# Performance work log

Hardware: AMD Instinct MI355X
Metric: run time of the kernel (lower is better)

The kernel has to match this reference:

```python
import jax, jax.numpy as jnp
import numpy as np

# Dims: B batch, CK key dim, CV value dim, NOBJ objects, T memory frames, HxW feature map
B, CK, CV, NOBJ, T, H, W = 1, 64, 512, 2, 2, 64, 64


def setup_inputs() -> dict:
    key = jax.random.key(0)
    k1, k2, k3, k4, k5 = jax.random.split(key, 5)
    return {
        "query_key": jax.random.normal(k1, (B, CK, H, W), jnp.float32),
        "query_selection": jax.random.uniform(k2, (B, CK, H, W), jnp.float32),
        "memory_key": jax.random.normal(k3, (B, CK, T, H, W), jnp.float32),
        "memory_shrinkage": jax.random.uniform(k4, (B, 1, T, H, W), jnp.float32),
        "memory_value": jax.random.normal(k5, (B, NOBJ, CV, T, H, W), jnp.float32),
    }


def reference(query_key, query_selection, memory_key, memory_shrinkage, memory_value):
    b, nobj, cv = memory_value.shape[:3]
    ck = memory_key.shape[1]
    h, w = query_key.shape[-2:]
    hw = h * w
    mk = memory_key.reshape(b, ck, -1)            # (b, ck, N) with N = T*H*W
    ms = memory_shrinkage.reshape(b, -1)          # (b, N)
    qk = query_key.reshape(b, ck, hw)             # (b, ck, hw)
    qe = query_selection.reshape(b, ck, hw)       # (b, ck, hw)
    mv = memory_value.reshape(b, nobj * cv, -1)   # (b, nobj*cv, N)

    # Negative L2 similarity with selection weighting (XMem get_similarity)
    a_sq = jnp.einsum('bcn,bcp->bnp', mk * mk, qe)            # (b, N, hw)
    two_ab = 2.0 * jnp.einsum('bcn,bcp->bnp', mk, qk * qe)    # (b, N, hw)
    b_sq = jnp.sum(qe * qk * qk, axis=1, keepdims=True)       # (b, 1, hw)
    inv_sqrt_ck = np.float32(1.0 / np.sqrt(ck))
    sim = (two_ab - a_sq - b_sq) * ms[:, :, None] * inv_sqrt_ck

    # Softmax over memory slots (dim N), then weighted readout
    aff = jax.nn.softmax(sim, axis=1)                          # (b, N, hw)
    mem = jnp.einsum('bvn,bnp->bvp', mv, aff)                  # (b, nobj*cv, hw)
    return mem.reshape(b, nobj, cv, h, w)
```

## Files before the change

kernel.cpp:

```cpp
#include <hip/hip_runtime.h>
#include <stdint.h>

typedef unsigned short u16;
typedef __attribute__((ext_vector_type(4))) float f32x4;
typedef __attribute__((ext_vector_type(8))) __bf16 bf16x8;
typedef __attribute__((ext_vector_type(4))) unsigned int u32x4;

#define HWPX 4096
#define NMEM 8192
#define CKD  64
#define VROWS 1024

__device__ __forceinline__ u16 f2bf(float x) {
    union { float f; unsigned u; } v; v.f = x;
    unsigned r = v.u + 0x7FFFu + ((v.u >> 16) & 1u);
    return (u16)(r >> 16);
}

__device__ __forceinline__ void gld_lds16(const void* g, void* l) {
    __builtin_amdgcn_global_load_lds(
        (const __attribute__((address_space(1))) uint32_t*)g,
        (__attribute__((address_space(3))) uint32_t*)l, 16, 0, 0);
}


__global__ void prep_qk(const float* __restrict__ qk, const float* __restrict__ qe,
                        const float* __restrict__ mk,
                        u16* __restrict__ Qf, float* __restrict__ bsq,
                        u16* __restrict__ Kf) {
    const int bx = blockIdx.x;
    const int tid = threadIdx.x;
    if (bx < 16) {
        int p = bx * 256 + tid;
        const int pt = p >> 7, wm = (p >> 6) & 1, mi = (p >> 4) & 3, l15 = p & 15;
        const size_t cb = ((((size_t)pt * 2 + 0) * 2 + wm) * 4 + mi) * 2;
        float acc = 0.f;
        #pragma unroll
        for (int cg = 0; cg < 8; ++cg) {
            const int kk = cg >> 2, quad = cg & 3;
            float kv[8], ev[8];
            #pragma unroll
            for (int j = 0; j < 8; ++j) {
                int c = cg * 8 + j;
                kv[j] = qk[c * HWPX + p];
                ev[j] = qe[c * HWPX + p];
                acc += ev[j] * kv[j] * kv[j];
            }
            unsigned w0[4], w1[4];
            #pragma unroll
            for (int jj = 0; jj < 4; ++jj) {
                w0[jj] = (unsigned)f2bf(kv[2*jj] * ev[2*jj]) |
                         ((unsigned)f2bf(kv[2*jj+1] * ev[2*jj+1]) << 16);
                w1[jj] = (unsigned)f2bf(ev[2*jj]) |
                         ((unsigned)f2bf(ev[2*jj+1]) << 16);
            }
            const size_t off = (size_t)quad * 128 + (size_t)l15 * 8;
            *(u32x4*)(Qf + (cb + kk) * 512 + off)      = (u32x4){w0[0], w0[1], w0[2], w0[3]};
            *(u32x4*)(Qf + (cb + 16 + kk) * 512 + off) = (u32x4){w1[0], w1[1], w1[2], w1[3]};
        }
        bsq[p] = acc;
    } else {
        int n = (bx - 16) * 256 + tid;
        const int nt = n >> 7, wn = (n >> 6) & 1, ni = (n >> 4) & 3, l15 = n & 15;
        const size_t cb = ((((size_t)nt * 2 + 0) * 2 + wn) * 4 + ni) * 2;
        #pragma unroll
        for (int cg = 0; cg < 8; ++cg) {
            const int kk = cg >> 2, quad = cg & 3;
            float m[8];
            #pragma unroll
            for (int j = 0; j < 8; ++j)
                m[j] = mk[(cg * 8 + j) * NMEM + n];
            unsigned w0[4], w1[4];
            #pragma unroll
            for (int jj = 0; jj < 4; ++jj) {
                w0[jj] = (unsigned)f2bf(2.f * m[2*jj]) |
                         ((unsigned)f2bf(2.f * m[2*jj+1]) << 16);
                w1[jj] = (unsigned)f2bf(-m[2*jj] * m[2*jj]) |
                         ((unsigned)f2bf(-m[2*jj+1] * m[2*jj+1]) << 16);
            }
            const size_t off = (size_t)quad * 128 + (size_t)l15 * 8;
            *(u32x4*)(Kf + (cb + kk) * 512 + off)      = (u32x4){w0[0], w0[1], w0[2], w0[3]};
            *(u32x4*)(Kf + (cb + 16 + kk) * 512 + off) = (u32x4){w1[0], w1[1], w1[2], w1[3]};
        }
    }
}

__launch_bounds__(256, 2)
__global__ void gemm1_combo(const u16* __restrict__ Qf, const u16* __restrict__ Kf,
                            const float* __restrict__ bsq, const float* __restrict__ ms,
                            const float* __restrict__ mv,
                            u16* __restrict__ Pt, float* __restrict__ dpart,
                            u16* __restrict__ mvb, float* __restrict__ outz) {
    const int blk = blockIdx.x;
    const int tid = threadIdx.x;

    if (blk < 512) {
        #pragma unroll 4
        for (int it = 0; it < 16; ++it) {
            int i = blk * 4096 + it * 256 + tid;
            float4 v = ((const float4*)mv)[i];
            u16 o0 = f2bf(v.x), o1 = f2bf(v.y), o2 = f2bf(v.z), o3 = f2bf(v.w);
            unsigned lo = (unsigned)o0 | ((unsigned)o1 << 16);
            unsigned hi = (unsigned)o2 | ((unsigned)o3 << 16);
            ((uint2*)mvb)[i] = make_uint2(lo, hi);
        }
        return;
    }
    if (blk < 768) {
        #pragma unroll 4
        for (int it = 0; it < 16; ++it) {
            int i = (blk - 512) * 4096 + it * 256 + tid;
            ((float4*)outz)[i] = make_float4(0.f, 0.f, 0.f, 0.f);
        }
        return;
    }

    __shared__ __align__(16) u16 smem[17408];

    const int tile = blk - 768;
    const int pb = tile & 31;
    const int nb = tile >> 5;
    const int p0 = pb * 128;
    const int n0 = nb * 128;

    const int l    = tid & 63;
    const int w    = tid >> 6;
    const int quad = l >> 4;
    const int l15  = l & 15;
    const int wm = w >> 1, wn = w & 1;

    f32x4 acc[4][4] = {};

    #pragma unroll
    for (int h = 0; h < 2; ++h) {
        bf16x8 a[4][2], b[4][2];
        const u16* qbase = Qf + ((((size_t)pb * 2 + h) * 2 + wm) * 4096) + (size_t)l * 8;
        const u16* kbase = Kf + ((((size_t)nb * 2 + h) * 2 + wn) * 4096) + (size_t)l * 8;
        #pragma unroll
        for (int mi = 0; mi < 4; ++mi) {
            a[mi][0] = *(const bf16x8*)(qbase + mi * 1024);
            a[mi][1] = *(const bf16x8*)(qbase + mi * 1024 + 512);
        }
        #pragma unroll
        for (int ni = 0; ni < 4; ++ni) {
            b[ni][0] = *(const bf16x8*)(kbase + ni * 1024);
            b[ni][1] = *(const bf16x8*)(kbase + ni * 1024 + 512);
        }
        #pragma unroll
        for (int kk = 0; kk < 2; ++kk)
            #pragma unroll
            for (int mi = 0; mi < 4; ++mi)
                #pragma unroll
                for (int ni = 0; ni < 4; ++ni)
                    acc[mi][ni] = __builtin_amdgcn_mfma_f32_16x16x32_bf16(a[mi][kk], b[ni][kk], acc[mi][ni], 0, 0, 0);
    }

    float msv[4];
    #pragma unroll
    for (int ni = 0; ni < 4; ++ni)
        msv[ni] = ms[n0 + wn * 64 + ni * 16 + l15] * 0.125f;
    float bsv[4][4];
    #pragma unroll
    for (int mi = 0; mi < 4; ++mi)
        #pragma unroll
        for (int r = 0; r < 4; ++r)
            bsv[mi][r] = bsq[p0 + wm * 64 + mi * 16 + quad * 4 + r];

    u16* Ps = smem;
    float rowsum[4][4] = {};
    #pragma unroll
    for (int mi = 0; mi < 4; ++mi) {
        #pragma unroll
        for (int ni = 0; ni < 4; ++ni) {
            f32x4 v = acc[mi][ni];
            int col = wn * 64 + ni * 16 + l15;
            #pragma unroll
            for (int r = 0; r < 4; ++r) {
                int rowl = wm * 64 + mi * 16 + quad * 4 + r;
                float pv = __expf((v[r] - bsv[mi][r]) * msv[ni]);
                rowsum[mi][r] += pv;
                Ps[rowl * 136 + col] = f2bf(pv);
            }
        }
    }
    #pragma unroll
    for (int mi = 0; mi < 4; ++mi)
        #pragma unroll
        for (int r = 0; r < 4; ++r) {
            float s = rowsum[mi][r];
            s += __shfl_xor(s, 1);
            s += __shfl_xor(s, 2);
            s += __shfl_xor(s, 4);
            s += __shfl_xor(s, 8);
            rowsum[mi][r] = s;
        }
    {
        float myv = 0.f;
        #pragma unroll
        for (int mi = 0; mi < 4; ++mi)
            #pragma unroll
            for (int r = 0; r < 4; ++r)
                if (l15 == mi * 4 + r) myv = rowsum[mi][r];
        int slice = nb * 2 + wn;
        dpart[(size_t)slice * HWPX + p0 + wm * 64 + (l15 >> 2) * 16 + quad * 4 + (l15 & 3)] = myv;
    }
    __syncthreads();

    {
        const size_t dstBase = (size_t)pb * 1048576 + (size_t)nb * 16384;
        #pragma unroll
        for (int it = 0; it < 8; ++it) {
            const int combo = it * 4 + w;
            const int kt  = combo >> 4;
            const int wnq = (combo >> 3) & 1;
            const int niq = (combo >> 1) & 3;
            const int kkq = combo & 1;
            const u32x4* src = (const u32x4*)(Ps + (wnq * 64 + niq * 16 + l15) * 136
                                                 + kt * 64 + kkq * 32 + quad * 8);
            u32x4* dst = (u32x4*)(Pt + dstBase + kt * 8192 + wnq * 4096
                                     + niq * 1024 + kkq * 512 + l * 8);
            *dst = *src;
        }
    }
}

__launch_bounds__(256, 3)
__global__ void gemm2_kernel(const u16* __restrict__ Ab, const u16* __restrict__ Btf,
                             const float* __restrict__ dpart, float* __restrict__ outacc) {
    __shared__ __align__(16) u16 As[128 * 64];

    const int tid  = threadIdx.x;
    const int l    = tid & 63;
    const int w    = tid >> 6;
    const int quad = l >> 4;
    const int l15  = l & 15;
    const int wm = w >> 1, wn = w & 1;

    const int lin = blockIdx.x + (blockIdx.y << 3) + (blockIdx.z << 8);
    const int vb  = (lin >> 3) & 7;
    const int pb  = (lin & 7) | (((lin >> 6) & 3) << 3);
    const int kz  = lin >> 8;
    const int v0 = vb * 128;
    const int p0 = pb * 128;
    const int kbeg = kz * (NMEM / 4);
    const int kend = kbeg + (NMEM / 4);

    const int rsub = tid >> 3;
    const int csw  = (tid & 7) ^ (rsub & 7);

    const u16* bbase = Btf + (size_t)pb * 1048576 + (size_t)wn * 4096 + (size_t)l * 8;

    f32x4 acc[4][4] = {};

    for (int k0 = kbeg; k0 < kend; k0 += 64) {
        const int kt = k0 >> 6;
        __syncthreads();
        #pragma unroll
        for (int rnd = 0; rnd < 4; ++rnd)
            gld_lds16(Ab + (size_t)(v0 + rnd * 32 + rsub) * NMEM + k0 + csw * 8,
                      As + rnd * 2048 + w * 512);
        bf16x8 b[4][2];
        {
            const u16* bk = bbase + (size_t)kt * 8192;
            #pragma unroll
            for (int ni = 0; ni < 4; ++ni) {
                b[ni][0] = *(const bf16x8*)(bk + ni * 1024);
                b[ni][1] = *(const bf16x8*)(bk + ni * 1024 + 512);
            }
        }
        __syncthreads();
        #pragma unroll
        for (int kk = 0; kk < 2; ++kk) {
            bf16x8 a[4];
            #pragma unroll
            for (int mi = 0; mi < 4; ++mi) {
                int row = wm * 64 + mi * 16 + l15;
                a[mi] = *(const bf16x8*)(As + row * 64 + (((kk * 4 + quad) ^ (l15 & 7)) << 3));
            }
            #pragma unroll
            for (int mi = 0; mi < 4; ++mi)
                #pragma unroll
                for (int ni = 0; ni < 4; ++ni)
                    acc[mi][ni] = __builtin_amdgcn_mfma_f32_16x16x32_bf16(a[mi], b[ni][kk], acc[mi][ni], 0, 0, 0);
        }
    }

    __syncthreads();
    float* dtmp  = (float*)As;
    float* dinvs = (float*)(As + 2048);
    {
        int p = tid & 127, h = tid >> 7;
        float s = 0.f;
        #pragma unroll 8
        for (int sl = 0; sl < 64; ++sl)
            s += dpart[(size_t)(h * 64 + sl) * HWPX + p0 + p];
        dtmp[tid] = s;
    }
    __syncthreads();
    if (tid < 128) dinvs[tid] = 1.0f / (dtmp[tid] + dtmp[tid + 128]);
    __syncthreads();

    float dinv[4];
    #pragma unroll
    for (int ni = 0; ni < 4; ++ni)
        dinv[ni] = dinvs[wn * 64 + ni * 16 + l15];

    #pragma unroll
    for (int mi = 0; mi < 4; ++mi) {
        #pragma unroll
        for (int ni = 0; ni < 4; ++ni) {
            int col = p0 + wn * 64 + ni * 16 + l15;
            f32x4 v = acc[mi][ni];
            #pragma unroll
            for (int r = 0; r < 4; ++r) {
                int row = v0 + wm * 64 + mi * 16 + quad * 4 + r;
                atomicAdd(&outacc[(size_t)row * HWPX + col], v[r] * dinv[ni]);
            }
        }
    }
}

extern "C" void kernel_launch(void* const* d_in, const int* in_sizes, int n_in,
                              void* d_out, int out_size, void* d_ws, size_t ws_size,
                              hipStream_t stream) {
    const float* qk = (const float*)d_in[0];
    const float* qe = (const float*)d_in[1];
    const float* mk = (const float*)d_in[2];
    const float* ms = (const float*)d_in[3];
    const float* mv = (const float*)d_in[4];
    float* out = (float*)d_out;

    char* ws = (char*)d_ws;
    u16*   Pt    = (u16*)ws;
    u16*   mvb   = (u16*)(ws + ((size_t)64 << 20));
    u16*   Kf    = (u16*)(ws + ((size_t)80 << 20));
    u16*   Qf    = (u16*)(ws + ((size_t)82 << 20));
    float* bsq   = (float*)(ws + ((size_t)83 << 20));
    float* dpart = (float*)(ws + ((size_t)83 << 20) + 65536);

    prep_qk<<<48, 256, 0, stream>>>(qk, qe, mk, Qf, bsq, Kf);

    gemm1_combo<<<2816, 256, 0, stream>>>(Qf, Kf, bsq, ms, mv, Pt, dpart, mvb, out);

    dim3 g2(8, 32, 4);
    gemm2_kernel<<<g2, 256, 0, stream>>>(mvb, Pt, dpart, out);
}
```

Measured before the change: 222.0 us.

## Move bf16 conversion to prep kernel, add denominator kernel, double gemm2 split-K

Moves the memory-value bf16 conversion and output zeroing from the gemm1 launch into the prep kernel, so gemm1 launches only its tiles. Adds a small kernel that reduces the softmax denominators once and stores their reciprocals, replacing the per-block reduction that every gemm2 block repeated. gemm2 now splits K eight ways instead of four, allows four blocks per CU, and uses plain block indexing. In exchange there is one more launch, twice as many atomic adds into the output, and the custom block-order swizzle that may have helped L2 reuse is gone.

Result: slower. 267.8 us (+20.6%).

```diff
diff --git a/kernel.cpp b/kernel.cpp
--- a/kernel.cpp
+++ b/kernel.cpp
@@ -24,10 +24,11 @@
 }
 
 
-__global__ void prep_qk(const float* __restrict__ qk, const float* __restrict__ qe,
-                        const float* __restrict__ mk,
-                        u16* __restrict__ Qf, float* __restrict__ bsq,
-                        u16* __restrict__ Kf) {
+__global__ void prep_aux(const float* __restrict__ qk, const float* __restrict__ qe,
+                         const float* __restrict__ mk, const float* __restrict__ mv,
+                         u16* __restrict__ Qf, float* __restrict__ bsq,
+                         u16* __restrict__ Kf, u16* __restrict__ mvb,
+                         float* __restrict__ outz) {
     const int bx = blockIdx.x;
     const int tid = threadIdx.x;
     if (bx < 16) {
@@ -59,7 +60,9 @@
             *(u32x4*)(Qf + (cb + 16 + kk) * 512 + off) = (u32x4){w1[0], w1[1], w1[2], w1[3]};
         }
         bsq[p] = acc;
-    } else {
+        return;
+    }
+    if (bx < 48) {
         int n = (bx - 16) * 256 + tid;
         const int nt = n >> 7, wn = (n >> 6) & 1, ni = (n >> 4) & 3, l15 = n & 15;
         const size_t cb = ((((size_t)nt * 2 + 0) * 2 + wn) * 4 + ni) * 2;
@@ -82,19 +85,10 @@
             *(u32x4*)(Kf + (cb + kk) * 512 + off)      = (u32x4){w0[0], w0[1], w0[2], w0[3]};
             *(u32x4*)(Kf + (cb + 16 + kk) * 512 + off) = (u32x4){w1[0], w1[1], w1[2], w1[3]};
         }
-    }
-}
-
-__launch_bounds__(256, 2)
-__global__ void gemm1_combo(const u16* __restrict__ Qf, const u16* __restrict__ Kf,
-                            const float* __restrict__ bsq, const float* __restrict__ ms,
-                            const float* __restrict__ mv,
-                            u16* __restrict__ Pt, float* __restrict__ dpart,
-                            u16* __restrict__ mvb, float* __restrict__ outz) {
-    const int blk = blockIdx.x;
-    const int tid = threadIdx.x;
-
-    if (blk < 512) {
+        return;
+    }
+    if (bx < 560) {
+        const int blk = bx - 48;
         #pragma unroll 4
         for (int it = 0; it < 16; ++it) {
             int i = blk * 4096 + it * 256 + tid;
@@ -106,23 +100,29 @@
         }
         return;
     }
-    if (blk < 768) {
+    {
+        const int blk = bx - 560;
         #pragma unroll 4
         for (int it = 0; it < 16; ++it) {
-            int i = (blk - 512) * 4096 + it * 256 + tid;
+            int i = blk * 4096 + it * 256 + tid;
             ((float4*)outz)[i] = make_float4(0.f, 0.f, 0.f, 0.f);
         }
-        return;
-    }
-
+    }
+}
+
+__launch_bounds__(256, 2)
+__global__ void gemm1_tiles(const u16* __restrict__ Qf, const u16* __restrict__ Kf,
+                            const float* __restrict__ bsq, const float* __restrict__ ms,
+                            u16* __restrict__ Pt, float* __restrict__ dpart) {
     __shared__ __align__(16) u16 smem[17408];
 
-    const int tile = blk - 768;
+    const int tile = blockIdx.x;
     const int pb = tile & 31;
     const int nb = tile >> 5;
     const int p0 = pb * 128;
     const int n0 = nb * 128;
 
+    const int tid  = threadIdx.x;
     const int l    = tid & 63;
     const int w    = tid >> 6;
     const int quad = l >> 4;
@@ -224,9 +224,18 @@
     }
 }
 
-__launch_bounds__(256, 3)
+__global__ void denom_kernel(const float* __restrict__ dpart, float* __restrict__ dinvg) {
+    const int p = blockIdx.x * 256 + threadIdx.x;
+    float s = 0.f;
+    #pragma unroll 8
+    for (int sl = 0; sl < 128; ++sl)
+        s += dpart[(size_t)sl * HWPX + p];
+    dinvg[p] = 1.0f / s;
+}
+
+__launch_bounds__(256, 4)
 __global__ void gemm2_kernel(const u16* __restrict__ Ab, const u16* __restrict__ Btf,
-                             const float* __restrict__ dpart, float* __restrict__ outacc) {
+                             const float* __restrict__ dinvg, float* __restrict__ outacc) {
     __shared__ __align__(16) u16 As[128 * 64];
 
     const int tid  = threadIdx.x;
@@ -236,14 +245,12 @@
     const int l15  = l & 15;
     const int wm = w >> 1, wn = w & 1;
 
-    const int lin = blockIdx.x + (blockIdx.y << 3) + (blockIdx.z << 8);
-    const int vb  = (lin >> 3) & 7;
-    const int pb  = (lin & 7) | (((lin >> 6) & 3) << 3);
-    const int kz  = lin >> 8;
+    const int vb = blockIdx.x;
+    const int pb = blockIdx.y;
+    const int kz = blockIdx.z;
     const int v0 = vb * 128;
     const int p0 = pb * 128;
-    const int kbeg = kz * (NMEM / 4);
-    const int kend = kbeg + (NMEM / 4);
+    const int kbeg = kz * (NMEM / 8);
 
     const int rsub = tid >> 3;
     const int csw  = (tid & 7) ^ (rsub & 7);
@@ -252,7 +259,8 @@
 
     f32x4 acc[4][4] = {};
 
-    for (int k0 = kbeg; k0 < kend; k0 += 64) {
+    for (int t = 0; t < 16; ++t) {
+        const int k0 = kbeg + t * 64;
         const int kt = k0 >> 6;
         __syncthreads();
         #pragma unroll
@@ -285,25 +293,10 @@
         }
     }
 
-    __syncthreads();
-    float* dtmp  = (float*)As;
-    float* dinvs = (float*)(As + 2048);
-    {
-        int p = tid & 127, h = tid >> 7;
-        float s = 0.f;
-        #pragma unroll 8
-        for (int sl = 0; sl < 64; ++sl)
-            s += dpart[(size_t)(h * 64 + sl) * HWPX + p0 + p];
-        dtmp[tid] = s;
-    }
-    __syncthreads();
-    if (tid < 128) dinvs[tid] = 1.0f / (dtmp[tid] + dtmp[tid + 128]);
-    __syncthreads();
-
     float dinv[4];
     #pragma unroll
     for (int ni = 0; ni < 4; ++ni)
-        dinv[ni] = dinvs[wn * 64 + ni * 16 + l15];
+        dinv[ni] = dinvg[p0 + wn * 64 + ni * 16 + l15];
 
     #pragma unroll
     for (int mi = 0; mi < 4; ++mi) {
@@ -337,11 +330,14 @@
     u16*   Qf    = (u16*)(ws + ((size_t)82 << 20));
     float* bsq   = (float*)(ws + ((size_t)83 << 20));
     float* dpart = (float*)(ws + ((size_t)83 << 20) + 65536);
-
-    prep_qk<<<48, 256, 0, stream>>>(qk, qe, mk, Qf, bsq, Kf);
-
-    gemm1_combo<<<2816, 256, 0, stream>>>(Qf, Kf, bsq, ms, mv, Pt, dpart, mvb, out);
-
-    dim3 g2(8, 32, 4);
-    gemm2_kernel<<<g2, 256, 0, stream>>>(mvb, Pt, dpart, out);
-}
+    float* dinvg = (float*)(ws + ((size_t)83 << 20) + 65536 + (2 << 20));
+
+    prep_aux<<<816, 256, 0, stream>>>(qk, qe, mk, mv, Qf, bsq, Kf, mvb, out);
+
+    gemm1_tiles<<<2048, 256, 0, stream>>>(Qf, Kf, bsq, ms, Pt, dpart);
+
+    denom_kernel<<<16, 256, 0, stream>>>(dpart, dinvg);
+
+    dim3 g2(8, 32, 8);
+    gemm2_kernel<<<g2, 256, 0, stream>>>(mvb, Pt, dinvg, out);
+}
```
